# Performance work log

Measured on AMD Instinct MI355X. Metric: run time of the kernel, lower is better.

## Reference

```python
import jax, jax.numpy as jnp
import numpy as np

VOCAB, EMB, HID, NCLS, B, T = 50000, 32, 64, 3, 512, 512

def setup_inputs() -> dict:
    key = jax.random.key(0)
    ks = jax.random.split(key, 7)
    tokens = jax.random.randint(ks[0], (B, T), 0, VOCAB, dtype=jnp.int32)
    emb = jax.random.normal(ks[1], (VOCAB, EMB), dtype=jnp.float32) * 0.05
    # Keras LSTM weights: kernel [EMB, 4*HID], recurrent_kernel [HID, 4*HID], bias [4*HID]; gate order i,f,c,o
    Wk = jax.random.normal(ks[2], (EMB, 4 * HID), dtype=jnp.float32) * (1.0 / np.sqrt(EMB))
    Wr = jax.random.normal(ks[3], (HID, 4 * HID), dtype=jnp.float32) * (1.0 / np.sqrt(HID))
    b = jnp.zeros((4 * HID,), dtype=jnp.float32)
    Wd = jax.random.normal(ks[4], (HID, NCLS), dtype=jnp.float32) * (1.0 / np.sqrt(HID))
    bd = jnp.zeros((NCLS,), dtype=jnp.float32)
    return {"tokens": tokens, "emb": emb, "Wk": Wk, "Wr": Wr, "b": b, "Wd": Wd, "bd": bd}

def _lstm_last_hidden(x, Wk, Wr, b):
    # x: [B, T, EMB] -> last hidden state [B, HID]. Keras gate order: i, f, c(g), o.
    Bsz = x.shape[0]
    # Precompute input projections for all timesteps (one big GEMM): [T, B, 4H]
    xz = jnp.einsum('bte,eh->tbh', x, Wk) + b

    def step(carry, xzt):
        h, c = carry
        z = xzt + h @ Wr  # [B, 4H]
        i, f, g, o = jnp.split(z, 4, axis=-1)
        i = jax.nn.sigmoid(i)
        f = jax.nn.sigmoid(f)
        o = jax.nn.sigmoid(o)
        c = f * c + i * jnp.tanh(g)
        h = o * jnp.tanh(c)
        return (h, c), None

    h0 = jnp.zeros((Bsz, HID), dtype=x.dtype)
    c0 = jnp.zeros((Bsz, HID), dtype=x.dtype)
    (hT, _), _ = jax.lax.scan(step, (h0, c0), xz)
    return hT

def reference(tokens, emb, Wk, Wr, b, Wd, bd):
    x = emb[tokens]                      # [B, T, EMB] embedding lookup
    h = _lstm_last_hidden(x, Wk, Wr, b)  # [B, HID]
    # Dropout layers are identity at inference; Dense + softmax
    logits = h @ Wd + bd                 # [B, NCLS]
    return jax.nn.softmax(logits, axis=-1)
```

## Files before the change

kernel.cpp:

```cpp
#include <hip/hip_runtime.h>


#define VOCAB 50000
#define EMB 32
#define HID 64
#define NCLS 3
#define BATCH 512
#define TSEQ 512
#define FOURH 256
#define LOG2E 1.4426950408889634f
#define GSEQ 4
#define NBLK (BATCH / GSEQ)

typedef _Float16 half8 __attribute__((ext_vector_type(8)));
typedef float f32x4 __attribute__((ext_vector_type(4)));

#define MFMA16 __builtin_amdgcn_mfma_f32_16x16x32_f16
#define PKRTZ(a, b) __builtin_bit_cast(int, __builtin_amdgcn_cvt_pkrtz((a), (b)))

#define WAVE_BARRIER()                                        \
    {                                                         \
        asm volatile("s_waitcnt lgkmcnt(0)" ::: "memory");    \
        __builtin_amdgcn_s_barrier();                         \
    }

__global__ __launch_bounds__(256)
void build_table(const float* __restrict__ emb, const float* __restrict__ Wk,
                 const float* __restrict__ bias, float* __restrict__ table) {
    const int c = threadIdx.x;
    const int u = c >> 2, g = c & 3;
    const int wi = (g << 6) + u;
    const float bb = bias[wi];
    float wcol[EMB];
#pragma unroll
    for (int k = 0; k < EMB; ++k) wcol[k] = Wk[k * FOURH + wi];
    for (int v = blockIdx.x; v < VOCAB; v += gridDim.x) {
        const float4* er = (const float4*)(emb + (long)v * EMB);
        float acc = bb;
#pragma unroll
        for (int kk = 0; kk < EMB / 4; ++kk) {
            const float4 e = er[kk];
            acc = fmaf(e.x, wcol[kk * 4 + 0], acc);
            acc = fmaf(e.y, wcol[kk * 4 + 1], acc);
            acc = fmaf(e.z, wcol[kk * 4 + 2], acc);
            acc = fmaf(e.w, wcol[kk * 4 + 3], acc);
        }
        table[(long)v * FOURH + c] = acc;
    }
}

#define LSTM_STEP(CUR, TT, ZX, TK, XW, XL)                                    \
    {                                                                         \
        const half8* ap = (const half8*)(hxc + (CUR) * 768 + abase);          \
        const half8 a0 = ap[0];                                               \
        const half8 a1 = ap[4];                                               \
        f32x4 ac0, ac1, ac2, ac3;                                             \
        if constexpr (TAB) {                                                  \
            ac0 = MFMA16(a0, bfr[0][0], ZX, 0, 0, 0);                         \
            ac1 = MFMA16(a0, bfr[1][0], ZX, 0, 0, 0);                         \
            ac2 = MFMA16(a0, bfr[2][0], ZX, 0, 0, 0);                         \
            ac3 = MFMA16(a0, bfr[3][0], ZX, 0, 0, 0);                         \
        } else {                                                              \
            ac0 = MFMA16(a0, bfr[0][0], zz, 0, 0, 0);                         \
            ac1 = MFMA16(a0, bfr[1][0], zz, 0, 0, 0);                         \
            ac2 = MFMA16(a0, bfr[2][0], zz, 0, 0, 0);                         \
            ac3 = MFMA16(a0, bfr[3][0], zz, 0, 0, 0);                         \
        }                                                                     \
        ac0 = MFMA16(a1, bfr[0][1], ac0, 0, 0, 0);                            \
        ac1 = MFMA16(a1, bfr[1][1], ac1, 0, 0, 0);                            \
        ac2 = MFMA16(a1, bfr[2][1], ac2, 0, 0, 0);                            \
        ac3 = MFMA16(a1, bfr[3][1], ac3, 0, 0, 0);                            \
        if constexpr (TAB) {                                                  \
            ZX = *(const f32x4*)(table + (long)(TK) * FOURH + (u << 2));      \
            const int tn4 = ((TT) + 4 < TSEQ) ? (TT) + 4 : TSEQ - 1;          \
            TK = toks[(q << 9) + tn4];                                        \
        } else {                                                              \
            const half8 a2 = ap[8];                                           \
            ac0 = MFMA16(a2, bfr[0][2], ac0, 0, 0, 0);                        \
            ac1 = MFMA16(a2, bfr[1][2], ac1, 0, 0, 0);                        \
            ac2 = MFMA16(a2, bfr[2][2], ac2, 0, 0, 0);                        \
            ac3 = MFMA16(a2, bfr[3][2], ac3, 0, 0, 0);                        \
            if (li8) {                                                        \
                int2 st;                                                      \
                st.x = PKRTZ(XW.x, XW.y);                                     \
                st.y = PKRTZ(XW.z, XW.w);                                     \
                *(int2*)(hxc + ((CUR) ^ 1) * 768 + xwoff) = st;               \
                const int tn2 = ((TT) + 2 < TSEQ) ? (TT) + 2 : TSEQ - 1;      \
                const int tk2 = toks[(w << 9) + tn2];                         \
                XL = *(const float4*)(emb + (long)tk2 * EMB + (l << 2));      \
            }                                                                 \
        }                                                                     \
        const float zi = ac0[0];                                              \
        const float zf = ac1[1];                                              \
        const float zg = ac2[2];                                              \
        const float zo = ac3[3];                                              \
        const float si = __builtin_amdgcn_rcpf(                               \
            1.0f + __builtin_amdgcn_exp2f(fmaf(zi, -LOG2E, bci)));            \
        const float sf = __builtin_amdgcn_rcpf(                               \
            1.0f + __builtin_amdgcn_exp2f(fmaf(zf, -LOG2E, bcf)));            \
        const float sg = __builtin_amdgcn_rcpf(                               \
            1.0f + __builtin_amdgcn_exp2f(fmaf(zg, -2.0f * LOG2E, bcg)));     \
        const float so = __builtin_amdgcn_rcpf(                               \
            1.0f + __builtin_amdgcn_exp2f(fmaf(zo, -LOG2E, bco)));            \
        const float gt = fmaf(2.0f, sg, -1.0f);                               \
        cst = fmaf(sf, cst, si * gt);                                         \
        const float st2 = __builtin_amdgcn_rcpf(                              \
            1.0f + __builtin_amdgcn_exp2f(cst * (-2.0f * LOG2E)));            \
        const float hv = so * fmaf(2.0f, st2, -1.0f);                         \
        *(_Float16*)(hxc + ((CUR) ^ 1) * 768 + hwoff) = (_Float16)hv;         \
        WAVE_BARRIER()                                                        \
    }

template <bool TAB>
__global__ __launch_bounds__(256)
void lstm_kernel(const int* __restrict__ tokens, const float* __restrict__ emb,
                 const float* __restrict__ Wk, const float* __restrict__ Wr,
                 const float* __restrict__ bias, const float* __restrict__ Wd,
                 const float* __restrict__ bd, const float* __restrict__ table,
                 float* __restrict__ out)
{
    __shared__ __align__(16) _Float16 hx[2][GSEQ][96];
    __shared__ int toks[GSEQ * TSEQ];

    const int tid = threadIdx.x;
    const int w   = tid >> 6;
    const int l   = tid & 63;
    const int li  = l & 15;
    const int q   = l >> 4;
    const bool li8 = (l < 8);
    const int s0  = blockIdx.x << 2;

    char* hxc = (char*)&hx[0][0][0];

    {
        const int4* src = (const int4*)(tokens + ((long)s0 << 9));
        int4* dst = (int4*)toks;
        dst[tid]       = src[tid];
        dst[tid + 256] = src[tid + 256];
    }

    if (tid < 64) {
        int2 z2; z2.x = 0; z2.y = 0;
        *(int2*)(hxc + (tid >> 4) * 192 + ((tid & 15) << 3)) = z2;
    }

    half8 bfr[4][3];
#pragma unroll
    for (int g = 0; g < 4; ++g) {
        const int col = (g << 6) + (w << 4) + li;
#pragma unroll
        for (int i = 0; i < 8; ++i) {
            const int kq = (q << 3) + i;
            bfr[g][0][i] = (_Float16)Wr[kq * FOURH + col];
            bfr[g][1][i] = (_Float16)Wr[(32 + kq) * FOURH + col];
            if constexpr (!TAB) bfr[g][2][i] = (_Float16)Wk[kq * FOURH + col];
        }
    }

    const int u = (w << 4) + li;
    const float bci = TAB ? 0.0f : -bias[u] * LOG2E;
    const float bcf = TAB ? 0.0f : -bias[u + 64] * LOG2E;
    const float bcg = TAB ? 0.0f : -bias[u + 128] * (2.0f * LOG2E);
    const float bco = TAB ? 0.0f : -bias[u + 192] * LOG2E;

    const int abase = ((li >> 2) * 192) + (q << 4);
    const int hwoff = q * 192 + (u << 1);
    const int xwoff = w * 192 + 128 + (l << 3);

    __syncthreads();

    f32x4 zxA{}, zxB{};
    int tkA = 0, tkB = 0;
    float4 xA = make_float4(0.f, 0.f, 0.f, 0.f);
    float4 xB = make_float4(0.f, 0.f, 0.f, 0.f);
    if constexpr (TAB) {
        const int t0 = toks[(q << 9) + 0];
        const int t1 = toks[(q << 9) + 1];
        zxA = *(const f32x4*)(table + (long)t0 * FOURH + (u << 2));
        zxB = *(const f32x4*)(table + (long)t1 * FOURH + (u << 2));
        tkA = toks[(q << 9) + 2];
        tkB = toks[(q << 9) + 3];
    } else {
        if (li8) {
            const int tk0 = toks[w << 9];
            const float4 x0 = *(const float4*)(emb + (long)tk0 * EMB + (l << 2));
            int2 st;
            st.x = PKRTZ(x0.x, x0.y);
            st.y = PKRTZ(x0.z, x0.w);
            *(int2*)(hxc + xwoff) = st;
            const int tk1 = toks[(w << 9) + 1];
            xA = *(const float4*)(emb + (long)tk1 * EMB + (l << 2));
        }
    }
    __syncthreads();

    float cst = 0.0f;
    const f32x4 zz = {0.0f, 0.0f, 0.0f, 0.0f};

    for (int t = 0; t < TSEQ; t += 2) {
        LSTM_STEP(0, t,     zxA, tkA, xA, xB)
        LSTM_STEP(1, t + 1, zxB, tkB, xB, xA)
    }

    if (tid < GSEQ) {
        const _Float16* hf = &hx[0][tid][0];
        float a0 = bd[0], a1 = bd[1], a2 = bd[2];
#pragma unroll 8
        for (int k = 0; k < HID; ++k) {
            const float hk = (float)hf[k];
            a0 = fmaf(hk, Wd[k * NCLS + 0], a0);
            a1 = fmaf(hk, Wd[k * NCLS + 1], a1);
            a2 = fmaf(hk, Wd[k * NCLS + 2], a2);
        }
        const float mm = fmaxf(a0, fmaxf(a1, a2));
        const float e0 = __expf(a0 - mm);
        const float e1 = __expf(a1 - mm);
        const float e2 = __expf(a2 - mm);
        const float den = e0 + e1 + e2;
        float* op = out + (s0 + tid) * NCLS;
        op[0] = e0 / den;
        op[1] = e1 / den;
        op[2] = e2 / den;
    }
}

extern "C" void kernel_launch(void* const* d_in, const int* in_sizes, int n_in,
                              void* d_out, int out_size, void* d_ws, size_t ws_size,
                              hipStream_t stream) {
    const int*   tokens = (const int*)  d_in[0];
    const float* emb    = (const float*)d_in[1];
    const float* Wk     = (const float*)d_in[2];
    const float* Wr     = (const float*)d_in[3];
    const float* b      = (const float*)d_in[4];
    const float* Wd     = (const float*)d_in[5];
    const float* bd     = (const float*)d_in[6];
    float* out = (float*)d_out;
    (void)in_sizes; (void)n_in; (void)out_size;

    const size_t need = (size_t)VOCAB * FOURH * sizeof(float);
    if (ws_size >= need) {
        float* table = (float*)d_ws;
        build_table<<<dim3(2048), dim3(256), 0, stream>>>(emb, Wk, b, table);
        lstm_kernel<true><<<dim3(NBLK), dim3(256), 0, stream>>>(
            tokens, emb, Wk, Wr, b, Wd, bd, table, out);
    } else {
        lstm_kernel<false><<<dim3(NBLK), dim3(256), 0, stream>>>(
            tokens, emb, Wk, Wr, b, Wd, bd, nullptr, out);
    }
}
```

Baseline: 201.3 us.

## Store precomputed gate table in fp16 and read tokens directly from global

The vocab×4H input-projection table is now written and read as fp16, which halves the build-kernel write traffic and the per-step gather bandwidth in the LSTM loop. The table gather and next-token fetch move ahead of the MFMAs, and tokens are read straight from global memory instead of being staged in LDS, which drops a staging copy and a barrier. The build grid is doubled. In exchange the precomputed gate pre-activations lose precision to fp16 rounding, and the per-step token reads now go to global/L1 rather than LDS.

```diff
diff --git a/kernel.cpp b/kernel.cpp
--- a/kernel.cpp
+++ b/kernel.cpp
@@ -13,6 +13,7 @@
 #define NBLK (BATCH / GSEQ)
 
 typedef _Float16 half8 __attribute__((ext_vector_type(8)));
+typedef _Float16 half4 __attribute__((ext_vector_type(4)));
 typedef float f32x4 __attribute__((ext_vector_type(4)));
 
 #define MFMA16 __builtin_amdgcn_mfma_f32_16x16x32_f16
@@ -26,7 +27,7 @@
 
 __global__ __launch_bounds__(256)
 void build_table(const float* __restrict__ emb, const float* __restrict__ Wk,
-                 const float* __restrict__ bias, float* __restrict__ table) {
+                 const float* __restrict__ bias, _Float16* __restrict__ table) {
     const int c = threadIdx.x;
     const int u = c >> 2, g = c & 3;
     const int wi = (g << 6) + u;
@@ -45,21 +46,30 @@
             acc = fmaf(e.z, wcol[kk * 4 + 2], acc);
             acc = fmaf(e.w, wcol[kk * 4 + 3], acc);
         }
-        table[(long)v * FOURH + c] = acc;
+        table[(long)v * FOURH + c] = (_Float16)acc;
     }
 }
 
-#define LSTM_STEP(CUR, TT, ZX, TK, XW, XL)                                    \
+#define LSTM_STEP(CUR, TT, ZR, TK, XW, XL)                                    \
     {                                                                         \
         const half8* ap = (const half8*)(hxc + (CUR) * 768 + abase);          \
         const half8 a0 = ap[0];                                               \
         const half8 a1 = ap[4];                                               \
         f32x4 ac0, ac1, ac2, ac3;                                             \
         if constexpr (TAB) {                                                  \
-            ac0 = MFMA16(a0, bfr[0][0], ZX, 0, 0, 0);                         \
-            ac1 = MFMA16(a0, bfr[1][0], ZX, 0, 0, 0);                         \
-            ac2 = MFMA16(a0, bfr[2][0], ZX, 0, 0, 0);                         \
-            ac3 = MFMA16(a0, bfr[3][0], ZX, 0, 0, 0);                         \
+            const half4 hz = __builtin_bit_cast(half4, ZR);                   \
+            f32x4 zx;                                                         \
+            zx[0] = (float)hz[0];                                             \
+            zx[1] = (float)hz[1];                                             \
+            zx[2] = (float)hz[2];                                             \
+            zx[3] = (float)hz[3];                                             \
+            ac0 = MFMA16(a0, bfr[0][0], zx, 0, 0, 0);                         \
+            ac1 = MFMA16(a0, bfr[1][0], zx, 0, 0, 0);                         \
+            ac2 = MFMA16(a0, bfr[2][0], zx, 0, 0, 0);                         \
+            ac3 = MFMA16(a0, bfr[3][0], zx, 0, 0, 0);                         \
+            ZR = *(const int2*)(tab16 + (long)(TK) * FOURH + (u << 2));       \
+            const int tn4 = ((TT) + 4 < TSEQ) ? (TT) + 4 : TSEQ - 1;          \
+            TK = tokq[tn4];                                                   \
         } else {                                                              \
             ac0 = MFMA16(a0, bfr[0][0], zz, 0, 0, 0);                         \
             ac1 = MFMA16(a0, bfr[1][0], zz, 0, 0, 0);                         \
@@ -70,11 +80,7 @@
         ac1 = MFMA16(a1, bfr[1][1], ac1, 0, 0, 0);                            \
         ac2 = MFMA16(a1, bfr[2][1], ac2, 0, 0, 0);                            \
         ac3 = MFMA16(a1, bfr[3][1], ac3, 0, 0, 0);                            \
-        if constexpr (TAB) {                                                  \
-            ZX = *(const f32x4*)(table + (long)(TK) * FOURH + (u << 2));      \
-            const int tn4 = ((TT) + 4 < TSEQ) ? (TT) + 4 : TSEQ - 1;          \
-            TK = toks[(q << 9) + tn4];                                        \
-        } else {                                                              \
+        if constexpr (!TAB) {                                                 \
             const half8 a2 = ap[8];                                           \
             ac0 = MFMA16(a2, bfr[0][2], ac0, 0, 0, 0);                        \
             ac1 = MFMA16(a2, bfr[1][2], ac1, 0, 0, 0);                        \
@@ -116,7 +122,7 @@
 void lstm_kernel(const int* __restrict__ tokens, const float* __restrict__ emb,
                  const float* __restrict__ Wk, const float* __restrict__ Wr,
                  const float* __restrict__ bias, const float* __restrict__ Wd,
-                 const float* __restrict__ bd, const float* __restrict__ table,
+                 const float* __restrict__ bd, const _Float16* __restrict__ tab16,
                  float* __restrict__ out)
 {
     __shared__ __align__(16) _Float16 hx[2][GSEQ][96];
@@ -132,7 +138,7 @@
 
     char* hxc = (char*)&hx[0][0][0];
 
-    {
+    if constexpr (!TAB) {
         const int4* src = (const int4*)(tokens + ((long)s0 << 9));
         int4* dst = (int4*)toks;
         dst[tid]       = src[tid];
@@ -167,19 +173,21 @@
     const int hwoff = q * 192 + (u << 1);
     const int xwoff = w * 192 + 128 + (l << 3);
 
+    const int* tokq = tokens + ((long)(s0 + q) << 9);
+
     __syncthreads();
 
-    f32x4 zxA{}, zxB{};
+    int2 zrA{}, zrB{};
     int tkA = 0, tkB = 0;
     float4 xA = make_float4(0.f, 0.f, 0.f, 0.f);
     float4 xB = make_float4(0.f, 0.f, 0.f, 0.f);
     if constexpr (TAB) {
-        const int t0 = toks[(q << 9) + 0];
-        const int t1 = toks[(q << 9) + 1];
-        zxA = *(const f32x4*)(table + (long)t0 * FOURH + (u << 2));
-        zxB = *(const f32x4*)(table + (long)t1 * FOURH + (u << 2));
-        tkA = toks[(q << 9) + 2];
-        tkB = toks[(q << 9) + 3];
+        const int t0 = tokq[0];
+        const int t1 = tokq[1];
+        zrA = *(const int2*)(tab16 + (long)t0 * FOURH + (u << 2));
+        zrB = *(const int2*)(tab16 + (long)t1 * FOURH + (u << 2));
+        tkA = tokq[2];
+        tkB = tokq[3];
     } else {
         if (li8) {
             const int tk0 = toks[w << 9];
@@ -191,15 +199,15 @@
             const int tk1 = toks[(w << 9) + 1];
             xA = *(const float4*)(emb + (long)tk1 * EMB + (l << 2));
         }
-    }
-    __syncthreads();
+        __syncthreads();
+    }
 
     float cst = 0.0f;
     const f32x4 zz = {0.0f, 0.0f, 0.0f, 0.0f};
 
     for (int t = 0; t < TSEQ; t += 2) {
-        LSTM_STEP(0, t,     zxA, tkA, xA, xB)
-        LSTM_STEP(1, t + 1, zxB, tkB, xB, xA)
+        LSTM_STEP(0, t,     zrA, tkA, xA, xB)
+        LSTM_STEP(1, t + 1, zrB, tkB, xB, xA)
     }
 
     if (tid < GSEQ) {
@@ -237,12 +245,12 @@
     float* out = (float*)d_out;
     (void)in_sizes; (void)n_in; (void)out_size;
 
-    const size_t need = (size_t)VOCAB * FOURH * sizeof(float);
+    const size_t need = (size_t)VOCAB * FOURH * sizeof(_Float16);
     if (ws_size >= need) {
-        float* table = (float*)d_ws;
-        build_table<<<dim3(2048), dim3(256), 0, stream>>>(emb, Wk, b, table);
+        _Float16* tab16 = (_Float16*)d_ws;
+        build_table<<<dim3(4096), dim3(256), 0, stream>>>(emb, Wk, b, tab16);
         lstm_kernel<true><<<dim3(NBLK), dim3(256), 0, stream>>>(
-            tokens, emb, Wk, Wr, b, Wd, bd, table, out);
+            tokens, emb, Wk, Wr, b, Wd, bd, tab16, out);
     } else {
         lstm_kernel<false><<<dim3(NBLK), dim3(256), 0, stream>>>(
             tokens, emb, Wk, Wr, b, Wd, bd, nullptr, out);
```

After: 233.9 us. 16.2% more time.
